# Kernel tuning notes

Hardware: AMD Instinct MI355X
Metric: run time of the kernel (lower is better)

The kernel has to match this reference:

```python
import jax, jax.numpy as jnp
import numpy as np

NUM_EMBED = 1024
NUM_HEADS = 16
BLOCK_SIZE = 2048


def setup_inputs() -> dict:
    key = jax.random.key(0)
    k1, k2, k3, k4, k5 = jax.random.split(key, 5)
    C = NUM_EMBED
    s = 1.0 / np.sqrt(C)
    x = jax.random.normal(k1, (2, BLOCK_SIZE, C), dtype=jnp.float32)
    # nn.Linear params: weight (out,in), bias (out,)
    w_attn = jax.random.uniform(k2, (3 * C, C), minval=-s, maxval=s, dtype=jnp.float32)
    b_attn = jax.random.uniform(k3, (3 * C,), minval=-s, maxval=s, dtype=jnp.float32)
    w_proj = jax.random.uniform(k4, (C, C), minval=-s, maxval=s, dtype=jnp.float32)
    b_proj = jax.random.uniform(k5, (C,), minval=-s, maxval=s, dtype=jnp.float32)
    return {"x": x, "w_attn": w_attn, "b_attn": b_attn, "w_proj": w_proj, "b_proj": b_proj}


def reference(x, w_attn, b_attn, w_proj, b_proj):
    B, T, C = x.shape
    H = NUM_HEADS
    D = C // H
    kqv = jnp.einsum('btc,oc->bto', x, w_attn) + b_attn  # (B,T,3C)
    # Original code splits as K, Q, V in that order.
    K, Q, V = jnp.split(kqv, 3, axis=2)
    K = K.reshape(B, T, H, D).transpose(0, 2, 1, 3)  # (B,H,T,D)
    Q = Q.reshape(B, T, H, D).transpose(0, 2, 1, 3)
    V = V.reshape(B, T, H, D).transpose(0, 2, 1, 3)
    aff = jnp.einsum('bhqd,bhkd->bhqk', Q, K) * (D ** -0.5)  # (B,H,T,T)
    causal = jnp.tril(jnp.ones((T, T), dtype=bool))
    aff = jnp.where(causal[None, None], aff, jnp.float32(-jnp.inf))
    wei = jax.nn.softmax(aff, axis=-1)
    attn = jnp.einsum('bhqk,bhkd->bhqd', wei, V)
    attn = attn.transpose(0, 2, 1, 3).reshape(B, T, C)
    out = jnp.einsum('btc,oc->bto', attn, w_proj) + b_proj
    return out
```

## Files before the change

kernel.cpp:

```cpp
#include <hip/hip_runtime.h>
#include <hip/hip_bf16.h>
#include <cstdint>

typedef __attribute__((ext_vector_type(8))) short bf16x8;
typedef __attribute__((ext_vector_type(4))) float f32x4;
typedef __attribute__((ext_vector_type(4))) uint16_t u16x4;

__device__ __forceinline__ uint16_t f2b(float f) {
  union { float f; uint32_t i; } v; v.f = f;
  return (uint16_t)((v.i + 0x7FFFu + ((v.i >> 16) & 1u)) >> 16);
}

#define GLDS16(g, l) __builtin_amdgcn_global_load_lds( \
    (const __attribute__((address_space(1))) void*)(g), \
    (__attribute__((address_space(3))) void*)(l), 16, 0, 0)

__global__ __launch_bounds__(256) void cvt_all(
    const float* __restrict__ x, const float* __restrict__ wa, const float* __restrict__ wp,
    uint16_t* __restrict__ xb, uint16_t* __restrict__ wab, uint16_t* __restrict__ wpb) {
  const int i = (blockIdx.x * 256 + threadIdx.x) * 4;
  const float* src; uint16_t* dst; int off;
  if (i < 4194304)      { src = x;  dst = xb;  off = i; }
  else if (i < 7340032) { src = wa; dst = wab; off = i - 4194304; }
  else                  { src = wp; dst = wpb; off = i - 7340032; }
  const float4 v = *(const float4*)(src + off);
  u16x4 o;
  o.x = f2b(v.x); o.y = f2b(v.y); o.z = f2b(v.z); o.w = f2b(v.w);
  *(u16x4*)(dst + off) = o;
}

template <int BM, bool OUT_BF16>
__global__ __launch_bounds__(256) void gemm_bt_bias(
    const uint16_t* __restrict__ A, const uint16_t* __restrict__ B,
    const float* __restrict__ bias, void* __restrict__ Cv,
    int M, int N, int K) {
  constexpr int MI = BM / 32;
  constexpr int CHA = BM / 16;
  constexpr int CPW = (CHA + 8) / 4;
  constexpr size_t ST_BYTES = (size_t)(BM + 128) * 32 * 2;
  constexpr size_t CT_BYTES = OUT_BF16 ? (size_t)4 * (BM / 2) * 72 * 2
                                       : (size_t)4 * (BM / 2) * 68 * 4;
  constexpr size_t LB = CT_BYTES > ST_BYTES ? CT_BYTES : ST_BYTES;
  __shared__ alignas(16) unsigned char ldsb[LB];
  uint16_t* lds = (uint16_t*)ldsb;
  const int offB = BM * 32;

  const int tid = threadIdx.x;
  const int wave = tid >> 6, lane = tid & 63;
  const int q4 = lane >> 4, l16 = lane & 15;
  const int wm = wave >> 1, wn = wave & 1;
  const long blockM = (long)blockIdx.y * BM;
  const long blockN = (long)blockIdx.x * 128;

  f32x4 acc[MI][4] = {};

  for (int k0 = 0; k0 < K; k0 += 32) {
#pragma unroll
    for (int c = 0; c < CPW; ++c) {
      const int id = c * 4 + wave;
      const bool isB = id >= CHA;
      const int a = isB ? id - CHA : id;
      const uint16_t* mat = isB ? B : A;
      const long rowBase = isB ? blockN : blockM;
      const int off = isB ? offB : 0;
      const int flat = a * 64 + lane;
      const int row = flat >> 2, seg = flat & 3;
      GLDS16(mat + (rowBase + row) * (long)K + k0 + seg * 8, lds + off + a * 512);
    }
    __syncthreads();
    bf16x8 af[MI], bfr[4];
#pragma unroll
    for (int i = 0; i < MI; ++i)
      af[i] = *(const bf16x8*)&lds[(wm * (BM / 2) + i * 16 + l16) * 32 + q4 * 8];
#pragma unroll
    for (int j = 0; j < 4; ++j)
      bfr[j] = *(const bf16x8*)&lds[offB + (wn * 64 + j * 16 + l16) * 32 + q4 * 8];
#pragma unroll
    for (int i = 0; i < MI; ++i)
#pragma unroll
      for (int j = 0; j < 4; ++j)
        acc[i][j] = __builtin_amdgcn_mfma_f32_16x16x32_bf16(af[i], bfr[j], acc[i][j], 0, 0, 0);
    __syncthreads();
  }

  if (OUT_BF16) {
    uint16_t* ct = lds + wave * (BM / 2) * 72;
#pragma unroll
    for (int j = 0; j < 4; ++j) {
      const float bv = bias[blockN + wn * 64 + j * 16 + l16];
#pragma unroll
      for (int i = 0; i < MI; ++i)
#pragma unroll
        for (int r = 0; r < 4; ++r)
          ct[(i * 16 + q4 * 4 + r) * 72 + j * 16 + l16] = f2b(acc[i][j][r] + bv);
    }
    __syncthreads();
    uint16_t* Cb = (uint16_t*)Cv;
#pragma unroll
    for (int st = 0; st < BM / 16; ++st) {
      const int flat = st * 64 + lane;
      const int row = flat >> 3, seg = flat & 7;
      const bf16x8 v = *(const bf16x8*)&ct[row * 72 + seg * 8];
      *(bf16x8*)&Cb[(blockM + wm * (BM / 2) + row) * (long)N + blockN + wn * 64 + seg * 8] = v;
    }
  } else {
    float* ct = (float*)ldsb + wave * (BM / 2) * 68;
#pragma unroll
    for (int j = 0; j < 4; ++j) {
      const float bv = bias[blockN + wn * 64 + j * 16 + l16];
#pragma unroll
      for (int i = 0; i < MI; ++i)
#pragma unroll
        for (int r = 0; r < 4; ++r)
          ct[(i * 16 + q4 * 4 + r) * 68 + j * 16 + l16] = acc[i][j][r] + bv;
    }
    __syncthreads();
    float* Cb = (float*)Cv;
#pragma unroll
    for (int st = 0; st < BM / 8; ++st) {
      const int flat = st * 64 + lane;
      const int row = flat >> 4, seg = flat & 15;
      const f32x4 v = *(const f32x4*)&ct[row * 68 + seg * 4];
      *(f32x4*)&Cb[(blockM + wm * (BM / 2) + row) * (long)N + blockN + wn * 64 + seg * 4] = v;
    }
  }
}

__global__ __launch_bounds__(256, 2) void attn_flash(
    const uint16_t* __restrict__ kqv, uint16_t* __restrict__ attn) {
  constexpr int T = 2048, C = 1024, C3 = 3072;
  __shared__ alignas(16) uint16_t Vt[2][64 * 136];
  __shared__ alignas(16) uint16_t Pt[2][4 * 2176];

  const int tid = threadIdx.x;
  const int wave = tid >> 6, lane = tid & 63;
  const int q4 = lane >> 4, l16 = lane & 15;
  const int p = blockIdx.x >> 5, bh = blockIdx.x & 31;
  const int b = bh >> 4, h = bh & 15;
  const size_t base = (size_t)b * T * C3;
  const size_t obase = (size_t)b * T * C;
  const int hD = h * 64;
  const float sc = 0.125f * 1.4426950408889634f;

  const int qb0 = 31 - p, qb1 = p;
  const int nkt0 = (qb0 >> 1) + 1;
  const int tr = tid >> 3, kch = tid & 7;

  int qb = qb0;
  int qrow = qb * 64 + wave * 16 + l16;
  bf16x8 qf0 = *(const bf16x8*)&kqv[base + (size_t)qrow * C3 + C + hD + q4 * 8];
  bf16x8 qf1 = *(const bf16x8*)&kqv[base + (size_t)qrow * C3 + C + hD + 32 + q4 * 8];

  f32x4 o[4] = {};
  float m_i = -1e30f, l_i = 0.f;
  int cb = 0, kt = 0;
  bool ss1 = false;

  bf16x8 pk[8][2], pv[2][2];
#pragma unroll
  for (int nk = 0; nk < 8; ++nk) {
    const uint16_t* kr = &kqv[base + (size_t)(nk * 16 + l16) * C3 + hD + q4 * 8];
    pk[nk][0] = *(const bf16x8*)kr;
    pk[nk][1] = *(const bf16x8*)(kr + 32);
  }
#pragma unroll
  for (int s2 = 0; s2 < 2; ++s2) {
    const size_t g = base + (size_t)(2 * (s2 * 32 + tr)) * C3 + 2 * C + hD + kch * 8;
    pv[s2][0] = *(const bf16x8*)&kqv[g];
    pv[s2][1] = *(const bf16x8*)&kqv[g + C3];
  }

  for (int t = 0; t < 17; ++t) {
    const int kbase = kt * 128;
    const bool lastOfStrip = !ss1 ? (kt == nkt0 - 1) : (t == 16);
    const int knext = lastOfStrip ? 0 : kt + 1;

    f32x4 s[8];
#pragma unroll
    for (int nk = 0; nk < 8; ++nk) {
      f32x4 z = {};
      z = __builtin_amdgcn_mfma_f32_16x16x32_bf16(pk[nk][0], qf0, z, 0, 0, 0);
      z = __builtin_amdgcn_mfma_f32_16x16x32_bf16(pk[nk][1], qf1, z, 0, 0, 0);
      s[nk] = z;
    }
    if (kbase + 127 > qb * 64 + wave * 16) {
#pragma unroll
      for (int nk = 0; nk < 8; ++nk) {
        const int key0 = kbase + nk * 16 + q4 * 4;
#pragma unroll
        for (int r = 0; r < 4; ++r)
          s[nk][r] = (key0 + r <= qrow) ? s[nk][r] : -1e30f;
      }
    }
    float mloc = s[0][0];
#pragma unroll
    for (int nk = 0; nk < 8; ++nk)
#pragma unroll
      for (int r = 0; r < 4; ++r) mloc = fmaxf(mloc, s[nk][r]);
    mloc = fmaxf(mloc, __shfl_xor(mloc, 16, 64));
    mloc = fmaxf(mloc, __shfl_xor(mloc, 32, 64));
    const float mnew = fmaxf(m_i, mloc * sc);
    const float alpha = exp2f(m_i - mnew);
    const bool mchg = mnew > m_i;
    m_i = mnew;
    float rs = 0.f;
#pragma unroll
    for (int nk = 0; nk < 8; ++nk)
#pragma unroll
      for (int r = 0; r < 4; ++r) {
        const float pe = exp2f(fmaf(s[nk][r], sc, -mnew));
        s[nk][r] = pe;
        rs += pe;
      }
    rs += __shfl_xor(rs, 16, 64);
    rs += __shfl_xor(rs, 32, 64);
    l_i = l_i * alpha + rs;
    if (__any(mchg)) {
#pragma unroll
      for (int r = 0; r < 4; ++r) {
        const float ar = __shfl(alpha, q4 * 4 + r, 64);
#pragma unroll
        for (int d4 = 0; d4 < 4; ++d4) o[d4][r] *= ar;
      }
    }
    {
      uint32_t* VtW = (uint32_t*)Vt[cb];
#pragma unroll
      for (int s2 = 0; s2 < 2; ++s2) {
        const int colw = ((s2 * 32 + tr) + 8 * kch) & 63;
        const uint32_t* a0 = (const uint32_t*)&pv[s2][0];
        const uint32_t* a1 = (const uint32_t*)&pv[s2][1];
#pragma unroll
        for (int i = 0; i < 8; ++i) {
          const uint32_t w = (i & 1)
              ? __builtin_amdgcn_perm(a1[i >> 1], a0[i >> 1], 0x07060302u)
              : __builtin_amdgcn_perm(a1[i >> 1], a0[i >> 1], 0x05040100u);
          VtW[(kch * 8 + i) * 68 + colw] = w;
        }
      }
    }
    uint16_t* Pw = &Pt[cb][wave * 2176];
#pragma unroll
    for (int nk = 0; nk < 8; ++nk) {
      union { __hip_bfloat162 h2; uint32_t u; } c01, c23;
      c01.h2 = __float22bfloat162_rn(make_float2(s[nk][0], s[nk][1]));
      c23.h2 = __float22bfloat162_rn(make_float2(s[nk][2], s[nk][3]));
      uint2 pkw; pkw.x = c01.u; pkw.y = c23.u;
      *(uint2*)&Pw[l16 * 136 + nk * 16 + q4 * 4] = pkw;
    }
    __syncthreads();
    if (t < 16) {
      const int kb2 = knext * 128;
#pragma unroll
      for (int nk = 0; nk < 8; ++nk) {
        const uint16_t* kr = &kqv[base + (size_t)(kb2 + nk * 16 + l16) * C3 + hD + q4 * 8];
        pk[nk][0] = *(const bf16x8*)kr;
        pk[nk][1] = *(const bf16x8*)(kr + 32);
      }
#pragma unroll
      for (int s2 = 0; s2 < 2; ++s2) {
        const size_t g = base + (size_t)(kb2 + 2 * (s2 * 32 + tr)) * C3 + 2 * C + hD + kch * 8;
        pv[s2][0] = *(const bf16x8*)&kqv[g];
        pv[s2][1] = *(const bf16x8*)&kqv[g + C3];
      }
    }
#pragma unroll
    for (int ks = 0; ks < 4; ++ks) {
      const bf16x8 pf = *(const bf16x8*)&Pw[l16 * 136 + ks * 32 + q4 * 8];
#pragma unroll
      for (int d4 = 0; d4 < 4; ++d4) {
        const int d = d4 * 16 + l16;
        const int col = (ks * 32 + q4 * 8 + 16 * (d >> 3)) & 127;
        const bf16x8 vf = *(const bf16x8*)&Vt[cb][d * 136 + col];
        o[d4] = __builtin_amdgcn_mfma_f32_16x16x32_bf16(pf, vf, o[d4], 0, 0, 0);
      }
    }
    if (lastOfStrip) {
      const float linv = 1.0f / l_i;
#pragma unroll
      for (int r = 0; r < 4; ++r) {
        const float lr = __shfl(linv, q4 * 4 + r, 64);
        const int q = qb * 64 + wave * 16 + q4 * 4 + r;
        const size_t rowoff = obase + (size_t)q * C + hD;
#pragma unroll
        for (int d4 = 0; d4 < 4; ++d4)
          attn[rowoff + d4 * 16 + l16] = f2b(o[d4][r] * lr);
      }
      if (!ss1) {
        ss1 = true;
        qb = qb1;
        qrow = qb * 64 + wave * 16 + l16;
        qf0 = *(const bf16x8*)&kqv[base + (size_t)qrow * C3 + C + hD + q4 * 8];
        qf1 = *(const bf16x8*)&kqv[base + (size_t)qrow * C3 + C + hD + 32 + q4 * 8];
#pragma unroll
        for (int d4 = 0; d4 < 4; ++d4) o[d4] = (f32x4){0.f, 0.f, 0.f, 0.f};
        m_i = -1e30f; l_i = 0.f;
        kt = 0;
      }
    } else {
      ++kt;
    }
    cb ^= 1;
  }
}

extern "C" void kernel_launch(void* const* d_in, const int* in_sizes, int n_in,
                              void* d_out, int out_size, void* d_ws, size_t ws_size,
                              hipStream_t stream) {
  const float* x      = (const float*)d_in[0];
  const float* w_attn = (const float*)d_in[1];
  const float* b_attn = (const float*)d_in[2];
  const float* w_proj = (const float*)d_in[3];
  const float* b_proj = (const float*)d_in[4];
  float* out = (float*)d_out;

  uint16_t* xb    = (uint16_t*)d_ws;
  uint16_t* wab   = xb  + (size_t)4096 * 1024;
  uint16_t* wpb   = wab + (size_t)3072 * 1024;
  uint16_t* kqv   = wpb + (size_t)1024 * 1024;
  uint16_t* attnb = kqv + (size_t)4096 * 3072;

  dim3 blk(256, 1, 1);
  hipLaunchKernelGGL(cvt_all, dim3(8192), blk, 0, stream, x, w_attn, w_proj, xb, wab, wpb);

  hipLaunchKernelGGL((gemm_bt_bias<128, true>), dim3(3072 / 128, 4096 / 128, 1), blk, 0, stream,
                     xb, wab, b_attn, (void*)kqv, 4096, 3072, 1024);
  hipLaunchKernelGGL(attn_flash, dim3(512, 1, 1), blk, 0, stream, kqv, attnb);
  hipLaunchKernelGGL((gemm_bt_bias<64, false>), dim3(1024 / 128, 4096 / 64, 1), blk, 0, stream,
                     attnb, wpb, b_proj, (void*)out, 4096, 1024, 1024);
}
```

Baseline: 219.4 us.

## Share K tile through LDS instead of per-wave redundant register loads

```diff
diff --git a/kernel.cpp b/kernel.cpp
--- a/kernel.cpp
+++ b/kernel.cpp
@@ -129,8 +129,10 @@
 __global__ __launch_bounds__(256, 2) void attn_flash(
     const uint16_t* __restrict__ kqv, uint16_t* __restrict__ attn) {
   constexpr int T = 2048, C = 1024, C3 = 3072;
-  __shared__ alignas(16) uint16_t Vt[2][64 * 136];
-  __shared__ alignas(16) uint16_t Pt[2][4 * 2176];
+  __shared__ alignas(16) uint16_t Kt[128 * 72];
+  __shared__ alignas(16) uint16_t Vt[64 * 136];
+  __shared__ alignas(16) uint16_t Pt[4][16 * 136];
+  uint32_t* VtW = (uint32_t*)Vt;
 
   const int tid = threadIdx.x;
   const int wave = tid >> 6, lane = tid & 63;
@@ -153,16 +155,13 @@
 
   f32x4 o[4] = {};
   float m_i = -1e30f, l_i = 0.f;
-  int cb = 0, kt = 0;
+  int kt = 0;
   bool ss1 = false;
 
-  bf16x8 pk[8][2], pv[2][2];
-#pragma unroll
-  for (int nk = 0; nk < 8; ++nk) {
-    const uint16_t* kr = &kqv[base + (size_t)(nk * 16 + l16) * C3 + hD + q4 * 8];
-    pk[nk][0] = *(const bf16x8*)kr;
-    pk[nk][1] = *(const bf16x8*)(kr + 32);
-  }
+  bf16x8 pk[4], pv[2][2];
+#pragma unroll
+  for (int rr = 0; rr < 4; ++rr)
+    pk[rr] = *(const bf16x8*)&kqv[base + (size_t)(rr * 32 + tr) * C3 + hD + kch * 8];
 #pragma unroll
   for (int s2 = 0; s2 < 2; ++s2) {
     const size_t g = base + (size_t)(2 * (s2 * 32 + tr)) * C3 + 2 * C + hD + kch * 8;
@@ -170,17 +169,50 @@
     pv[s2][1] = *(const bf16x8*)&kqv[g + C3];
   }
 
+  uint16_t* Pw = &Pt[wave][0];
+
   for (int t = 0; t < 17; ++t) {
     const int kbase = kt * 128;
     const bool lastOfStrip = !ss1 ? (kt == nkt0 - 1) : (t == 16);
-    const int knext = lastOfStrip ? 0 : kt + 1;
-
+
+    __syncthreads();
+#pragma unroll
+    for (int rr = 0; rr < 4; ++rr)
+      *(bf16x8*)&Kt[(rr * 32 + tr) * 72 + kch * 8] = pk[rr];
+#pragma unroll
+    for (int s2 = 0; s2 < 2; ++s2) {
+      const int colw = ((s2 * 32 + tr) + 8 * kch) & 63;
+      const uint32_t* a0 = (const uint32_t*)&pv[s2][0];
+      const uint32_t* a1 = (const uint32_t*)&pv[s2][1];
+#pragma unroll
+      for (int i = 0; i < 8; ++i) {
+        const uint32_t w = (i & 1)
+            ? __builtin_amdgcn_perm(a1[i >> 1], a0[i >> 1], 0x07060302u)
+            : __builtin_amdgcn_perm(a1[i >> 1], a0[i >> 1], 0x05040100u);
+        VtW[(kch * 8 + i) * 68 + colw] = w;
+      }
+    }
+    __syncthreads();
+    if (t < 16) {
+      const int kb2 = (lastOfStrip ? 0 : kt + 1) * 128;
+#pragma unroll
+      for (int rr = 0; rr < 4; ++rr)
+        pk[rr] = *(const bf16x8*)&kqv[base + (size_t)(kb2 + rr * 32 + tr) * C3 + hD + kch * 8];
+#pragma unroll
+      for (int s2 = 0; s2 < 2; ++s2) {
+        const size_t g = base + (size_t)(kb2 + 2 * (s2 * 32 + tr)) * C3 + 2 * C + hD + kch * 8;
+        pv[s2][0] = *(const bf16x8*)&kqv[g];
+        pv[s2][1] = *(const bf16x8*)&kqv[g + C3];
+      }
+    }
     f32x4 s[8];
 #pragma unroll
     for (int nk = 0; nk < 8; ++nk) {
       f32x4 z = {};
-      z = __builtin_amdgcn_mfma_f32_16x16x32_bf16(pk[nk][0], qf0, z, 0, 0, 0);
-      z = __builtin_amdgcn_mfma_f32_16x16x32_bf16(pk[nk][1], qf1, z, 0, 0, 0);
+      const bf16x8 kf0 = *(const bf16x8*)&Kt[(nk * 16 + l16) * 72 + q4 * 8];
+      const bf16x8 kf1 = *(const bf16x8*)&Kt[(nk * 16 + l16) * 72 + 32 + q4 * 8];
+      z = __builtin_amdgcn_mfma_f32_16x16x32_bf16(kf0, qf0, z, 0, 0, 0);
+      z = __builtin_amdgcn_mfma_f32_16x16x32_bf16(kf1, qf1, z, 0, 0, 0);
       s[nk] = z;
     }
     if (kbase + 127 > qb * 64 + wave * 16) {
@@ -223,23 +255,6 @@
         for (int d4 = 0; d4 < 4; ++d4) o[d4][r] *= ar;
       }
     }
-    {
-      uint32_t* VtW = (uint32_t*)Vt[cb];
-#pragma unroll
-      for (int s2 = 0; s2 < 2; ++s2) {
-        const int colw = ((s2 * 32 + tr) + 8 * kch) & 63;
-        const uint32_t* a0 = (const uint32_t*)&pv[s2][0];
-        const uint32_t* a1 = (const uint32_t*)&pv[s2][1];
-#pragma unroll
-        for (int i = 0; i < 8; ++i) {
-          const uint32_t w = (i & 1)
-              ? __builtin_amdgcn_perm(a1[i >> 1], a0[i >> 1], 0x07060302u)
-              : __builtin_amdgcn_perm(a1[i >> 1], a0[i >> 1], 0x05040100u);
-          VtW[(kch * 8 + i) * 68 + colw] = w;
-        }
-      }
-    }
-    uint16_t* Pw = &Pt[cb][wave * 2176];
 #pragma unroll
     for (int nk = 0; nk < 8; ++nk) {
       union { __hip_bfloat162 h2; uint32_t u; } c01, c23;
@@ -248,22 +263,6 @@
       uint2 pkw; pkw.x = c01.u; pkw.y = c23.u;
       *(uint2*)&Pw[l16 * 136 + nk * 16 + q4 * 4] = pkw;
     }
-    __syncthreads();
-    if (t < 16) {
-      const int kb2 = knext * 128;
-#pragma unroll
-      for (int nk = 0; nk < 8; ++nk) {
-        const uint16_t* kr = &kqv[base + (size_t)(kb2 + nk * 16 + l16) * C3 + hD + q4 * 8];
-        pk[nk][0] = *(const bf16x8*)kr;
-        pk[nk][1] = *(const bf16x8*)(kr + 32);
-      }
-#pragma unroll
-      for (int s2 = 0; s2 < 2; ++s2) {
-        const size_t g = base + (size_t)(kb2 + 2 * (s2 * 32 + tr)) * C3 + 2 * C + hD + kch * 8;
-        pv[s2][0] = *(const bf16x8*)&kqv[g];
-        pv[s2][1] = *(const bf16x8*)&kqv[g + C3];
-      }
-    }
 #pragma unroll
     for (int ks = 0; ks < 4; ++ks) {
       const bf16x8 pf = *(const bf16x8*)&Pw[l16 * 136 + ks * 32 + q4 * 8];
@@ -271,7 +270,7 @@
       for (int d4 = 0; d4 < 4; ++d4) {
         const int d = d4 * 16 + l16;
         const int col = (ks * 32 + q4 * 8 + 16 * (d >> 3)) & 127;
-        const bf16x8 vf = *(const bf16x8*)&Vt[cb][d * 136 + col];
+        const bf16x8 vf = *(const bf16x8*)&Vt[d * 136 + col];
         o[d4] = __builtin_amdgcn_mfma_f32_16x16x32_bf16(pf, vf, o[d4], 0, 0, 0);
       }
     }
@@ -300,7 +299,6 @@
     } else {
       ++kt;
     }
-    cb ^= 1;
   }
 }
 
```

New measurement: 198.9 us. 9.4% less time.
